# Performance work log

Hardware: AMD Instinct MI355X
Metric: run time of the kernel (lower is better)

## Reference

```python
import jax, jax.numpy as jnp
import numpy as np

NUM_USERS = 50000
NUM_ITEMS = 50000
N_NODES = NUM_USERS + NUM_ITEMS
DIM_FEAT = 256
HID = 128
EMB = 128
K = 3
N_EDGES = 1_600_000


def setup_inputs() -> dict:
    key = jax.random.key(0)
    ks = jax.random.split(key, 16)

    def xavier(k, shape):
        fan_in, fan_out = shape[-2], shape[-1]
        std = float(np.sqrt(2.0 / (fan_in + fan_out)))
        return jax.random.normal(k, shape, dtype=jnp.float32) * std

    return {
        "feat": jax.random.normal(ks[0], (NUM_ITEMS, DIM_FEAT), dtype=jnp.float32),
        "node_emb": jax.random.normal(ks[1], (N_NODES, EMB), dtype=jnp.float32),
        "src": jax.random.randint(ks[2], (N_EDGES,), 0, N_NODES, dtype=jnp.int32),
        "dst": jax.random.randint(ks[3], (N_EDGES,), 0, N_NODES, dtype=jnp.int32),
        "user_feat_emb": xavier(ks[4], (NUM_USERS, HID)),
        "trans_w": xavier(ks[5], (DIM_FEAT, HID)),
        "trans_b": jnp.zeros((HID,), dtype=jnp.float32),
        # layer 0: hidden->hidden; layers 1,2: emb->emb. hidden==emb so stack.
        "ws": xavier(ks[6], (K, HID, HID)),
        "des_w": xavier(ks[7], (K, HID, EMB)),
        "des_b": jnp.zeros((K, EMB), dtype=jnp.float32),
        # concat=True: outs[i] takes [h | u] of width hidden+emb
        "out_w": xavier(ks[8], (K, HID + EMB, EMB)),
        "out_b": jnp.zeros((K, EMB), dtype=jnp.float32),
    }


def reference(feat, node_emb, src, dst, user_feat_emb,
              trans_w, trans_b, ws, des_w, des_b, out_w, out_b):
    # feat = trans(feat); concat user embeddings; L2-normalize rows
    x = feat @ trans_w + trans_b                      # [num_items, HID]
    x = jnp.concatenate([user_feat_emb, x], axis=0)   # [N, HID]
    norm = jnp.linalg.norm(x, axis=1, keepdims=True)
    x = x / jnp.maximum(norm, 1e-12)

    lrelu = jax.nn.leaky_relu  # slope 0.01, matches F.leaky_relu default
    for i in range(K):
        # g.func(x, W): sparse adjacency aggregation (sum over in-edges) then dense W
        agg = jax.ops.segment_sum(x[src], dst, num_segments=N_NODES)  # [N, HID]
        h = lrelu(agg @ ws[i])                                        # [N, HID]
        u = lrelu(h @ des_w[i] + des_b[i] + node_emb)                 # [N, EMB]
        x = lrelu(jnp.concatenate([h, u], axis=1) @ out_w[i] + out_b[i])
    return x, user_feat_emb
```

## Files before the change

kernel.cpp:

```cpp
#include <hip/hip_runtime.h>

#define NN 100000
#define NU 50000
#define NI 50000
#define NE 1600000
#define NSLICE 5
#define SLICEW 20000

typedef unsigned short u16;
typedef unsigned int u32;

typedef __attribute__((ext_vector_type(8))) short s16x8;
typedef __attribute__((ext_vector_type(4))) float f32x4;
typedef __attribute__((ext_vector_type(4))) unsigned short us4;

__device__ __forceinline__ float bf2f(u16 u){
  union { u32 i; float f; } v; v.i = ((u32)u) << 16; return v.f;
}
__device__ __forceinline__ u16 f2bf(float f){
  union { float f; u32 i; } v; v.f = f;
  u32 u = v.i;
  return (u16)((u + 0x7FFFu + ((u >> 16) & 1u)) >> 16);
}
__device__ __forceinline__ u32 pack2(float lo, float hi){
  return (u32)f2bf(lo) | ((u32)f2bf(hi) << 16);
}
__device__ __forceinline__ float lrelu(float x){ return x > 0.f ? x : 0.01f * x; }
__device__ __forceinline__ float san(float v){
  union { float f; u32 i; } u; u.f = v;
  return ((u.i & 0x7F800000u) == 0x7F800000u) ? 0.f : v;
}

__global__ __launch_bounds__(256) void transpose_weights(
    const float* __restrict__ trans_w, const float* __restrict__ wsw,
    const float* __restrict__ desw, const float* __restrict__ outw,
    u16* __restrict__ Ttw, u16* __restrict__ Tw, u16* __restrict__ Td, u16* __restrict__ To)
{
  __shared__ u16 L[128][136];
  int b = blockIdx.x, t = threadIdx.x;
  const float* src; u16* dst; int stride;
  if (b < 2)      { src = trans_w + b*16384;        dst = Ttw + b*128;          stride = 256; }
  else if (b < 5) { int i = b-2; src = wsw  + i*16384; dst = Tw + i*16384;      stride = 128; }
  else if (b < 8) { int i = b-5; src = desw + i*16384; dst = Td + i*16384;      stride = 128; }
  else            { int i = (b-8)>>1, h = (b-8)&1;
                    src = outw + i*32768 + h*16384;    dst = To + i*32768 + h*128; stride = 256; }
  #pragma unroll
  for (int p = 0; p < 8; p++){
    int fi = (p*256 + t)*8;
    int r = fi >> 7, c = fi & 127;
    f32x4 v0 = *(const f32x4*)(src + r*128 + c);
    f32x4 v1 = *(const f32x4*)(src + r*128 + c + 4);
    L[c+0][r] = f2bf(san(v0.x)); L[c+1][r] = f2bf(san(v0.y));
    L[c+2][r] = f2bf(san(v0.z)); L[c+3][r] = f2bf(san(v0.w));
    L[c+4][r] = f2bf(san(v1.x)); L[c+5][r] = f2bf(san(v1.y));
    L[c+6][r] = f2bf(san(v1.z)); L[c+7][r] = f2bf(san(v1.w));
  }
  __syncthreads();
  #pragma unroll
  for (int p = 0; p < 8; p++){
    int fi = (p*256 + t)*8;
    int n = fi >> 7, k = fi & 127;
    us4 o0, o1;
    o0.x = L[n][k+0]; o0.y = L[n][k+1]; o0.z = L[n][k+2]; o0.w = L[n][k+3];
    o1.x = L[n][k+4]; o1.y = L[n][k+5]; o1.z = L[n][k+6]; o1.w = L[n][k+7];
    *(us4*)(dst + (size_t)n*stride + k)     = o0;
    *(us4*)(dst + (size_t)n*stride + k + 4) = o1;
  }
}

__global__ __launch_bounds__(256) void norm_users(const float* __restrict__ ufe, u16* __restrict__ X)
{
  int gid = blockIdx.x*256 + threadIdx.x;
  int row = gid >> 6, lane = gid & 63;
  float2 v = *(const float2*)(ufe + (size_t)row*128 + lane*2);
  float a = san(v.x), b = san(v.y);
  float ss = a*a + b*b;
  #pragma unroll
  for (int off = 32; off; off >>= 1) ss += __shfl_xor(ss, off, 64);
  float inv = 1.0f / fmaxf(sqrtf(ss), 1e-12f);
  *(u32*)(X + (size_t)row*128 + lane*2) = pack2(a*inv, b*inv);
}

__global__ __launch_bounds__(256) void trans_items(
    const float* __restrict__ feat, const u16* __restrict__ Ttw,
    const float* __restrict__ tb, u16* __restrict__ X)
{
  __shared__ u16 Af[128][136];
  __shared__ u16 Wl[128][136];
  __shared__ float rowss[128][9];
  __shared__ float rnorm[128];

  int t = threadIdx.x;
  int r0 = blockIdx.x * 128;
  int w = t >> 6, lane = t & 63;
  int l15 = lane & 15, q = lane >> 4;
  int m0 = (w & 1) * 64, n0 = (w >> 1) * 64;

  f32x4 acc[4][4];
  #pragma unroll
  for (int mi = 0; mi < 4; mi++)
    #pragma unroll
    for (int ni = 0; ni < 4; ni++){ acc[mi][ni].x = 0.f; acc[mi][ni].y = 0.f; acc[mi][ni].z = 0.f; acc[mi][ni].w = 0.f; }

  for (int half = 0; half < 2; half++){
    __syncthreads();
    #pragma unroll
    for (int p = 0; p < 8; p++){
      int fi = (p*256 + t)*8;
      int r = fi >> 7, c = fi & 127;
      int row = r0 + r;
      us4 o0 = {0,0,0,0}, o1 = {0,0,0,0};
      if (row < NI){
        f32x4 v0 = *(const f32x4*)(feat + (size_t)row*256 + half*128 + c);
        f32x4 v1 = *(const f32x4*)(feat + (size_t)row*256 + half*128 + c + 4);
        o0.x = f2bf(san(v0.x)); o0.y = f2bf(san(v0.y)); o0.z = f2bf(san(v0.z)); o0.w = f2bf(san(v0.w));
        o1.x = f2bf(san(v1.x)); o1.y = f2bf(san(v1.y)); o1.z = f2bf(san(v1.z)); o1.w = f2bf(san(v1.w));
      }
      *(us4*)&Af[r][c]     = o0;
      *(us4*)&Af[r][c + 4] = o1;
      *(us4*)&Wl[r][c]     = *(const us4*)(Ttw + (size_t)r*256 + half*128 + c);
      *(us4*)&Wl[r][c + 4] = *(const us4*)(Ttw + (size_t)r*256 + half*128 + c + 4);
    }
    __syncthreads();
    #pragma unroll
    for (int kc = 0; kc < 128; kc += 32){
      s16x8 afr[4], bfr[4];
      #pragma unroll
      for (int mi = 0; mi < 4; mi++) afr[mi] = *(const s16x8*)&Wl[m0 + 16*mi + l15][kc + 8*q];
      #pragma unroll
      for (int ni = 0; ni < 4; ni++) bfr[ni] = *(const s16x8*)&Af[n0 + 16*ni + l15][kc + 8*q];
      #pragma unroll
      for (int mi = 0; mi < 4; mi++)
        #pragma unroll
        for (int ni = 0; ni < 4; ni++)
          acc[mi][ni] = __builtin_amdgcn_mfma_f32_16x16x32_bf16(afr[mi], bfr[ni], acc[mi][ni], 0, 0, 0);
    }
  }

  float bias[4][4];
  #pragma unroll
  for (int mi = 0; mi < 4; mi++){
    int c0 = m0 + 16*mi + 4*q;
    f32x4 bv = *(const f32x4*)(tb + c0);
    bias[mi][0] = san(bv.x); bias[mi][1] = san(bv.y); bias[mi][2] = san(bv.z); bias[mi][3] = san(bv.w);
  }
  #pragma unroll
  for (int ni = 0; ni < 4; ni++){
    float ss = 0.f;
    #pragma unroll
    for (int mi = 0; mi < 4; mi++){
      float v0 = acc[mi][ni].x + bias[mi][0];
      float v1 = acc[mi][ni].y + bias[mi][1];
      float v2 = acc[mi][ni].z + bias[mi][2];
      float v3 = acc[mi][ni].w + bias[mi][3];
      ss += v0*v0 + v1*v1 + v2*v2 + v3*v3;
    }
    rowss[n0 + 16*ni + l15][(w & 1)*4 + q] = ss;
  }
  __syncthreads();
  if (t < 128){
    float s = 0.f;
    #pragma unroll
    for (int j = 0; j < 8; j++) s += rowss[t][j];
    rnorm[t] = 1.0f / fmaxf(sqrtf(s), 1e-12f);
  }
  __syncthreads();
  #pragma unroll
  for (int mi = 0; mi < 4; mi++){
    int c0 = m0 + 16*mi + 4*q;
    #pragma unroll
    for (int ni = 0; ni < 4; ni++){
      int r = n0 + 16*ni + l15;
      int row = r0 + r;
      if (row < NI){
        float inv = rnorm[r];
        us4 o;
        o.x = f2bf((acc[mi][ni].x + bias[mi][0]) * inv);
        o.y = f2bf((acc[mi][ni].y + bias[mi][1]) * inv);
        o.z = f2bf((acc[mi][ni].z + bias[mi][2]) * inv);
        o.w = f2bf((acc[mi][ni].w + bias[mi][3]) * inv);
        *(us4*)(X + (size_t)(NU + row)*128 + c0) = o;
      }
    }
  }
}

__global__ void zero_int(int* __restrict__ p, int n){
  int i = blockIdx.x*256 + threadIdx.x;
  if (i < n) p[i] = 0;
}
__global__ void hist_k(const int* __restrict__ dst, int* __restrict__ counts){
  int e = blockIdx.x*256 + threadIdx.x;
  if (e < NE){
    int d = dst[e];
    d = min(max(d, 0), NN - 1);
    atomicAdd(&counts[d], 1);
  }
}
__global__ __launch_bounds__(1024) void scan_k(const int* __restrict__ counts, int* __restrict__ row_ptr){
  __shared__ int lds[1024];
  __shared__ int carry;
  int t = threadIdx.x;
  if (t == 0) carry = 0;
  __syncthreads();
  for (int base = 0; base < NN; base += 4096){
    int idx = base + t*4;
    int4 v = {0,0,0,0};
    if (idx < NN) v = *(const int4*)(counts + idx);
    int s = v.x + v.y + v.z + v.w;
    lds[t] = s;
    __syncthreads();
    for (int off = 1; off < 1024; off <<= 1){
      int add = (t >= off) ? lds[t - off] : 0;
      __syncthreads();
      lds[t] += add;
      __syncthreads();
    }
    int incl = lds[t];
    int total = lds[1023];
    int run = carry;
    if (idx < NN){
      int e0 = run + incl - s;
      int4 o;
      o.x = e0; o.y = e0 + v.x; o.z = o.y + v.y; o.w = o.z + v.z;
      *(int4*)(row_ptr + idx) = o;
    }
    __syncthreads();
    if (t == 0) carry = run + total;
    __syncthreads();
  }
}

__global__ __launch_bounds__(256) void fill_slice(
    const int* __restrict__ src, const int* __restrict__ dst,
    int* __restrict__ row_ptr, int* __restrict__ esrc, int d0, int d1)
{
  int e = blockIdx.x*256 + threadIdx.x;
  if (e < NE){
    int d = dst[e];
    if (d >= d0 && d < d1){
      d = min(max(d, 0), NN - 1);
      int pos = atomicAdd(&row_ptr[d], 1);
      pos = min(max(pos, 0), NE - 1);
      esrc[pos] = src[e];
    }
  }
}

__global__ __launch_bounds__(256) void aggregate(
    const u16* __restrict__ X, const int* __restrict__ row_ptr,
    const int* __restrict__ esrc, u16* __restrict__ AGG)
{
  int gid = blockIdx.x*256 + threadIdx.x;
  int v = gid >> 6, lane = gid & 63;
  int sub = lane >> 4, li = lane & 15;
  int jb = (v == 0) ? 0 : row_ptr[v - 1];
  int je = row_ptr[v];
  jb = min(max(jb, 0), NE);
  je = min(max(je, jb), NE);

  float a0=0.f,a1=0.f,a2=0.f,a3=0.f,a4=0.f,a5=0.f,a6=0.f,a7=0.f;

  int j = jb + sub;
  for (; j + 4 < je; j += 8){
    int s0 = esrc[j];     s0 = min(max(s0, 0), NN - 1);
    int s1 = esrc[j + 4]; s1 = min(max(s1, 0), NN - 1);
    uint4 p0 = *(const uint4*)(X + (size_t)s0*128 + li*8);
    uint4 p1 = *(const uint4*)(X + (size_t)s1*128 + li*8);
    a0 += bf2f((u16)(p0.x & 0xFFFF)); a1 += bf2f((u16)(p0.x >> 16));
    a2 += bf2f((u16)(p0.y & 0xFFFF)); a3 += bf2f((u16)(p0.y >> 16));
    a4 += bf2f((u16)(p0.z & 0xFFFF)); a5 += bf2f((u16)(p0.z >> 16));
    a6 += bf2f((u16)(p0.w & 0xFFFF)); a7 += bf2f((u16)(p0.w >> 16));
    a0 += bf2f((u16)(p1.x & 0xFFFF)); a1 += bf2f((u16)(p1.x >> 16));
    a2 += bf2f((u16)(p1.y & 0xFFFF)); a3 += bf2f((u16)(p1.y >> 16));
    a4 += bf2f((u16)(p1.z & 0xFFFF)); a5 += bf2f((u16)(p1.z >> 16));
    a6 += bf2f((u16)(p1.w & 0xFFFF)); a7 += bf2f((u16)(p1.w >> 16));
  }
  for (; j < je; j += 4){
    int s0 = esrc[j]; s0 = min(max(s0, 0), NN - 1);
    uint4 p0 = *(const uint4*)(X + (size_t)s0*128 + li*8);
    a0 += bf2f((u16)(p0.x & 0xFFFF)); a1 += bf2f((u16)(p0.x >> 16));
    a2 += bf2f((u16)(p0.y & 0xFFFF)); a3 += bf2f((u16)(p0.y >> 16));
    a4 += bf2f((u16)(p0.z & 0xFFFF)); a5 += bf2f((u16)(p0.z >> 16));
    a6 += bf2f((u16)(p0.w & 0xFFFF)); a7 += bf2f((u16)(p0.w >> 16));
  }

  a0 += __shfl_xor(a0, 16, 64); a0 += __shfl_xor(a0, 32, 64);
  a1 += __shfl_xor(a1, 16, 64); a1 += __shfl_xor(a1, 32, 64);
  a2 += __shfl_xor(a2, 16, 64); a2 += __shfl_xor(a2, 32, 64);
  a3 += __shfl_xor(a3, 16, 64); a3 += __shfl_xor(a3, 32, 64);
  a4 += __shfl_xor(a4, 16, 64); a4 += __shfl_xor(a4, 32, 64);
  a5 += __shfl_xor(a5, 16, 64); a5 += __shfl_xor(a5, 32, 64);
  a6 += __shfl_xor(a6, 16, 64); a6 += __shfl_xor(a6, 32, 64);
  a7 += __shfl_xor(a7, 16, 64); a7 += __shfl_xor(a7, 32, 64);

  if (sub == 0){
    uint4 o;
    o.x = pack2(a0, a1); o.y = pack2(a2, a3);
    o.z = pack2(a4, a5); o.w = pack2(a6, a7);
    *(uint4*)(AGG + (size_t)v*128 + li*8) = o;
  }
}

__global__ __launch_bounds__(256, 2) void layer_fused(
    const u16* __restrict__ AGG, const float* __restrict__ nembF,
    const u16* __restrict__ Twi, const u16* __restrict__ Tdi,
    const float* __restrict__ dbF, const u16* __restrict__ Toi,
    const float* __restrict__ obF, u16* __restrict__ XoutB,
    float* __restrict__ XoutF, int last)
{
  __shared__ u16 Ab[128][136];
  __shared__ u16 Hb[128][136];

  int t = threadIdx.x;
  int r0 = blockIdx.x * 128;
  int w = t >> 6, lane = t & 63;
  int l15 = lane & 15, q = lane >> 4;
  int m0 = (w & 1) * 64, n0 = (w >> 1) * 64;

  f32x4 acc[4][4];

#define ZERO_ACC() \
  { _Pragma("unroll") for (int mi = 0; mi < 4; mi++) \
      { _Pragma("unroll") for (int ni = 0; ni < 4; ni++) \
        { acc[mi][ni].x = 0.f; acc[mi][ni].y = 0.f; acc[mi][ni].z = 0.f; acc[mi][ni].w = 0.f; } } }

#define GEMMG(BARR, WBASE, WSTRIDE, WKOFF) \
  { s16x8 afr[4][4]; \
    _Pragma("unroll") for (int mi = 0; mi < 4; mi++) \
      { _Pragma("unroll") for (int kk = 0; kk < 4; kk++) \
          afr[mi][kk] = *(const s16x8*)((WBASE) + (size_t)(m0 + 16*mi + l15)*(WSTRIDE) + (WKOFF) + kk*32 + 8*q); } \
    _Pragma("unroll") for (int kk = 0; kk < 4; kk++){ \
      s16x8 bfr[4]; \
      _Pragma("unroll") for (int ni = 0; ni < 4; ni++) bfr[ni] = *(const s16x8*)&BARR[n0 + 16*ni + l15][kk*32 + 8*q]; \
      _Pragma("unroll") for (int mi = 0; mi < 4; mi++) \
        { _Pragma("unroll") for (int ni = 0; ni < 4; ni++) \
          acc[mi][ni] = __builtin_amdgcn_mfma_f32_16x16x32_bf16(afr[mi][kk], bfr[ni], acc[mi][ni], 0, 0, 0); } } }

  #pragma unroll
  for (int p = 0; p < 8; p++){
    int fi = (p*256 + t)*8;
    int r = fi >> 7, c = fi & 127;
    int row = r0 + r;
    us4 o0 = {0,0,0,0}, o1 = {0,0,0,0};
    if (row < NN){
      o0 = *(const us4*)(AGG + (size_t)row*128 + c);
      o1 = *(const us4*)(AGG + (size_t)row*128 + c + 4);
    }
    *(us4*)&Ab[r][c]     = o0;
    *(us4*)&Ab[r][c + 4] = o1;
  }
  __syncthreads();

  ZERO_ACC();
  GEMMG(Ab, Twi, 128, 0);

  #pragma unroll
  for (int mi = 0; mi < 4; mi++){
    #pragma unroll
    for (int ni = 0; ni < 4; ni++){
      us4 o;
      o.x = f2bf(lrelu(acc[mi][ni].x));
      o.y = f2bf(lrelu(acc[mi][ni].y));
      o.z = f2bf(lrelu(acc[mi][ni].z));
      o.w = f2bf(lrelu(acc[mi][ni].w));
      *(us4*)&Hb[n0 + 16*ni + l15][m0 + 16*mi + 4*q] = o;
    }
  }
  __syncthreads();

  ZERO_ACC();
  GEMMG(Hb, Tdi, 128, 0);

  #pragma unroll
  for (int mi = 0; mi < 4; mi++){
    int c0 = m0 + 16*mi + 4*q;
    f32x4 dbv = *(const f32x4*)(dbF + c0);
    float db0 = san(dbv.x), db1 = san(dbv.y), db2 = san(dbv.z), db3 = san(dbv.w);
    #pragma unroll
    for (int ni = 0; ni < 4; ni++){
      int r = n0 + 16*ni + l15;
      int row = r0 + r;
      float e0 = 0.f, e1 = 0.f, e2 = 0.f, e3 = 0.f;
      if (row < NN){
        f32x4 nev = *(const f32x4*)(nembF + (size_t)row*128 + c0);
        e0 = san(nev.x); e1 = san(nev.y); e2 = san(nev.z); e3 = san(nev.w);
      }
      us4 o;
      o.x = f2bf(lrelu(acc[mi][ni].x + db0 + e0));
      o.y = f2bf(lrelu(acc[mi][ni].y + db1 + e1));
      o.z = f2bf(lrelu(acc[mi][ni].z + db2 + e2));
      o.w = f2bf(lrelu(acc[mi][ni].w + db3 + e3));
      *(us4*)&Ab[r][c0] = o;
    }
  }
  __syncthreads();

  ZERO_ACC();
  GEMMG(Hb, Toi, 256, 0);
  GEMMG(Ab, Toi, 256, 128);

  #pragma unroll
  for (int mi = 0; mi < 4; mi++){
    int c0 = m0 + 16*mi + 4*q;
    f32x4 obv = *(const f32x4*)(obF + c0);
    float b0 = san(obv.x), b1 = san(obv.y), b2 = san(obv.z), b3 = san(obv.w);
    #pragma unroll
    for (int ni = 0; ni < 4; ni++){
      int r = n0 + 16*ni + l15;
      int row = r0 + r;
      if (row < NN){
        if (last){
          f32x4 o;
          o.x = lrelu(acc[mi][ni].x + b0);
          o.y = lrelu(acc[mi][ni].y + b1);
          o.z = lrelu(acc[mi][ni].z + b2);
          o.w = lrelu(acc[mi][ni].w + b3);
          *(f32x4*)(XoutF + (size_t)row*128 + c0) = o;
        } else {
          us4 o;
          o.x = f2bf(lrelu(acc[mi][ni].x + b0));
          o.y = f2bf(lrelu(acc[mi][ni].y + b1));
          o.z = f2bf(lrelu(acc[mi][ni].z + b2));
          o.w = f2bf(lrelu(acc[mi][ni].w + b3));
          *(us4*)(XoutB + (size_t)row*128 + c0) = o;
        }
      }
    }
  }
#undef ZERO_ACC
#undef GEMMG
}

__global__ void copy_ufe(const float4* __restrict__ s, float4* __restrict__ d, int n){
  int i = blockIdx.x*256 + threadIdx.x;
  if (i < n){
    float4 v = s[i];
    v.x = san(v.x); v.y = san(v.y); v.z = san(v.z); v.w = san(v.w);
    d[i] = v;
  }
}

extern "C" void kernel_launch(void* const* d_in, const int* in_sizes, int n_in,
                              void* d_out, int out_size, void* d_ws, size_t ws_size,
                              hipStream_t stream)
{
  const float* feat = (const float*)d_in[0];
  const float* nemb = (const float*)d_in[1];
  const int*   src  = (const int*)d_in[2];
  const int*   dst  = (const int*)d_in[3];
  const float* ufe  = (const float*)d_in[4];
  const float* tw   = (const float*)d_in[5];
  const float* tb   = (const float*)d_in[6];
  const float* wsw  = (const float*)d_in[7];
  const float* desw = (const float*)d_in[8];
  const float* desb = (const float*)d_in[9];
  const float* outw = (const float*)d_in[10];
  const float* outb = (const float*)d_in[11];

  float* out  = (float*)d_out;
  float* outU = out + (size_t)NN*128;

  u16* X = (u16*)out;

  char* p = (char*)d_ws;
  u16*   AGG = (u16*)p;    p += (size_t)NN*128*2;
  u16*   Ttw = (u16*)p;    p += (size_t)2*16384*2;
  u16*   Tw  = (u16*)p;    p += (size_t)3*16384*2;
  u16*   Td  = (u16*)p;    p += (size_t)3*16384*2;
  u16*   To  = (u16*)p;    p += (size_t)3*32768*2;
  int* row_ptr = (int*)p;  p += (size_t)100004*4;
  int* counts  = (int*)p;  p += (size_t)100000*4;
  int* esrc    = (int*)p;  p += (size_t)NE*4;

  transpose_weights<<<14, 256, 0, stream>>>(tw, wsw, desw, outw, Ttw, Tw, Td, To);
  norm_users<<<NU/4, 256, 0, stream>>>(ufe, X);
  trans_items<<<(NI + 127)/128, 256, 0, stream>>>(feat, Ttw, tb, X);

  zero_int<<<(NN + 255)/256, 256, 0, stream>>>(counts, NN);
  hist_k<<<(NE + 255)/256, 256, 0, stream>>>(dst, counts);
  scan_k<<<1, 1024, 0, stream>>>(counts, row_ptr);
  for (int s = 0; s < NSLICE; s++){
    fill_slice<<<(NE + 255)/256, 256, 0, stream>>>(src, dst, row_ptr, esrc,
        s*SLICEW, (s == NSLICE-1) ? NN : (s+1)*SLICEW);
  }

  for (int i = 0; i < 3; i++){
    aggregate<<<NN/4, 256, 0, stream>>>(X, row_ptr, esrc, AGG);
    layer_fused<<<(NN + 127)/128, 256, 0, stream>>>(AGG, nemb,
        Tw + (size_t)i*16384, Td + (size_t)i*16384, desb + (size_t)i*128,
        To + (size_t)i*32768, outb + (size_t)i*128, X, out, (i == 2) ? 1 : 0);
  }
  copy_ufe<<<(NU*128/4 + 255)/256, 256, 0, stream>>>((const float4*)ufe, (float4*)outU, NU*128/4);
}
```

Before: 782.5 us.

## Shrink GEMM row tiles, pre-convert node_emb to bf16, warp-scan, deeper gather unroll

Several independent changes. layer_fused and trans_items now use 64-row tiles with launch bounds of 4 blocks, and trans_items reads weight fragments straight from global memory instead of staging them in LDS; this lowers LDS and register use so more blocks fit per CU. node_emb is converted once to bf16 into the user-output region, so each layer reads half the bytes, at the cost of bf16 rounding on that term. The scan kernel replaces its barrier-heavy LDS Hillis-Steele loop with wave shuffles, and the aggregate gather loop is unrolled to four outstanding row loads.

```diff
diff --git a/kernel.cpp b/kernel.cpp
--- a/kernel.cpp
+++ b/kernel.cpp
@@ -68,6 +68,20 @@
   }
 }
 
+__global__ __launch_bounds__(256) void conv_nemb(
+    const float* __restrict__ nemb, u16* __restrict__ nembB)
+{
+  int i = blockIdx.x*256 + threadIdx.x;
+  size_t off = (size_t)i * 8;
+  f32x4 v0 = *(const f32x4*)(nemb + off);
+  f32x4 v1 = *(const f32x4*)(nemb + off + 4);
+  us4 o0, o1;
+  o0.x = f2bf(san(v0.x)); o0.y = f2bf(san(v0.y)); o0.z = f2bf(san(v0.z)); o0.w = f2bf(san(v0.w));
+  o1.x = f2bf(san(v1.x)); o1.y = f2bf(san(v1.y)); o1.z = f2bf(san(v1.z)); o1.w = f2bf(san(v1.w));
+  *(us4*)(nembB + off)     = o0;
+  *(us4*)(nembB + off + 4) = o1;
+}
+
 __global__ __launch_bounds__(256) void norm_users(const float* __restrict__ ufe, u16* __restrict__ X)
 {
   int gid = blockIdx.x*256 + threadIdx.x;
@@ -81,31 +95,30 @@
   *(u32*)(X + (size_t)row*128 + lane*2) = pack2(a*inv, b*inv);
 }
 
-__global__ __launch_bounds__(256) void trans_items(
+__global__ __launch_bounds__(256, 4) void trans_items(
     const float* __restrict__ feat, const u16* __restrict__ Ttw,
     const float* __restrict__ tb, u16* __restrict__ X)
 {
-  __shared__ u16 Af[128][136];
-  __shared__ u16 Wl[128][136];
-  __shared__ float rowss[128][9];
-  __shared__ float rnorm[128];
+  __shared__ u16 Af[64][136];
+  __shared__ float rowss[64][8];
+  __shared__ float rnorm[64];
 
   int t = threadIdx.x;
-  int r0 = blockIdx.x * 128;
+  int r0 = blockIdx.x * 64;
   int w = t >> 6, lane = t & 63;
   int l15 = lane & 15, q = lane >> 4;
-  int m0 = (w & 1) * 64, n0 = (w >> 1) * 64;
-
-  f32x4 acc[4][4];
+  int m0 = (w & 1) * 64, n0 = (w >> 1) * 32;
+
+  f32x4 acc[4][2];
   #pragma unroll
   for (int mi = 0; mi < 4; mi++)
     #pragma unroll
-    for (int ni = 0; ni < 4; ni++){ acc[mi][ni].x = 0.f; acc[mi][ni].y = 0.f; acc[mi][ni].z = 0.f; acc[mi][ni].w = 0.f; }
+    for (int ni = 0; ni < 2; ni++){ acc[mi][ni].x = 0.f; acc[mi][ni].y = 0.f; acc[mi][ni].z = 0.f; acc[mi][ni].w = 0.f; }
 
   for (int half = 0; half < 2; half++){
     __syncthreads();
     #pragma unroll
-    for (int p = 0; p < 8; p++){
+    for (int p = 0; p < 4; p++){
       int fi = (p*256 + t)*8;
       int r = fi >> 7, c = fi & 127;
       int row = r0 + r;
@@ -118,21 +131,20 @@
       }
       *(us4*)&Af[r][c]     = o0;
       *(us4*)&Af[r][c + 4] = o1;
-      *(us4*)&Wl[r][c]     = *(const us4*)(Ttw + (size_t)r*256 + half*128 + c);
-      *(us4*)&Wl[r][c + 4] = *(const us4*)(Ttw + (size_t)r*256 + half*128 + c + 4);
     }
     __syncthreads();
     #pragma unroll
     for (int kc = 0; kc < 128; kc += 32){
-      s16x8 afr[4], bfr[4];
+      s16x8 afr[4], bfr[2];
       #pragma unroll
-      for (int mi = 0; mi < 4; mi++) afr[mi] = *(const s16x8*)&Wl[m0 + 16*mi + l15][kc + 8*q];
+      for (int mi = 0; mi < 4; mi++)
+        afr[mi] = *(const s16x8*)(Ttw + (size_t)(m0 + 16*mi + l15)*256 + half*128 + kc + 8*q);
       #pragma unroll
-      for (int ni = 0; ni < 4; ni++) bfr[ni] = *(const s16x8*)&Af[n0 + 16*ni + l15][kc + 8*q];
+      for (int ni = 0; ni < 2; ni++) bfr[ni] = *(const s16x8*)&Af[n0 + 16*ni + l15][kc + 8*q];
       #pragma unroll
       for (int mi = 0; mi < 4; mi++)
         #pragma unroll
-        for (int ni = 0; ni < 4; ni++)
+        for (int ni = 0; ni < 2; ni++)
           acc[mi][ni] = __builtin_amdgcn_mfma_f32_16x16x32_bf16(afr[mi], bfr[ni], acc[mi][ni], 0, 0, 0);
     }
   }
@@ -145,7 +157,7 @@
     bias[mi][0] = san(bv.x); bias[mi][1] = san(bv.y); bias[mi][2] = san(bv.z); bias[mi][3] = san(bv.w);
   }
   #pragma unroll
-  for (int ni = 0; ni < 4; ni++){
+  for (int ni = 0; ni < 2; ni++){
     float ss = 0.f;
     #pragma unroll
     for (int mi = 0; mi < 4; mi++){
@@ -158,7 +170,7 @@
     rowss[n0 + 16*ni + l15][(w & 1)*4 + q] = ss;
   }
   __syncthreads();
-  if (t < 128){
+  if (t < 64){
     float s = 0.f;
     #pragma unroll
     for (int j = 0; j < 8; j++) s += rowss[t][j];
@@ -169,7 +181,7 @@
   for (int mi = 0; mi < 4; mi++){
     int c0 = m0 + 16*mi + 4*q;
     #pragma unroll
-    for (int ni = 0; ni < 4; ni++){
+    for (int ni = 0; ni < 2; ni++){
       int r = n0 + 16*ni + l15;
       int row = r0 + r;
       if (row < NI){
@@ -198,35 +210,44 @@
   }
 }
 __global__ __launch_bounds__(1024) void scan_k(const int* __restrict__ counts, int* __restrict__ row_ptr){
-  __shared__ int lds[1024];
-  __shared__ int carry;
+  __shared__ int wsum[16];
+  __shared__ int woff[16];
+  __shared__ int tot;
   int t = threadIdx.x;
-  if (t == 0) carry = 0;
-  __syncthreads();
+  int lane = t & 63, wid = t >> 6;
+  int carry = 0;
   for (int base = 0; base < NN; base += 4096){
     int idx = base + t*4;
     int4 v = {0,0,0,0};
     if (idx < NN) v = *(const int4*)(counts + idx);
-    int s = v.x + v.y + v.z + v.w;
-    lds[t] = s;
+    int s4 = v.x + v.y + v.z + v.w;
+    int s = s4;
+    #pragma unroll
+    for (int off = 1; off < 64; off <<= 1){
+      int u = __shfl_up(s, off, 64);
+      if (lane >= off) s += u;
+    }
+    if (lane == 63) wsum[wid] = s;
     __syncthreads();
-    for (int off = 1; off < 1024; off <<= 1){
-      int add = (t >= off) ? lds[t - off] : 0;
-      __syncthreads();
-      lds[t] += add;
-      __syncthreads();
-    }
-    int incl = lds[t];
-    int total = lds[1023];
-    int run = carry;
+    if (t < 16){
+      int ws = wsum[t];
+      int wscan = ws;
+      #pragma unroll
+      for (int off = 1; off < 16; off <<= 1){
+        int u = __shfl_up(wscan, off, 64);
+        if (t >= off) wscan += u;
+      }
+      woff[t] = wscan - ws;
+      if (t == 15) tot = wscan;
+    }
+    __syncthreads();
     if (idx < NN){
-      int e0 = run + incl - s;
+      int e0 = carry + woff[wid] + (s - s4);
       int4 o;
       o.x = e0; o.y = e0 + v.x; o.z = o.y + v.y; o.w = o.z + v.z;
       *(int4*)(row_ptr + idx) = o;
     }
-    __syncthreads();
-    if (t == 0) carry = run + total;
+    carry += tot;
     __syncthreads();
   }
 }
@@ -247,6 +268,12 @@
   }
 }
 
+#define ACC8(P) \
+  a0 += bf2f((u16)(P.x & 0xFFFF)); a1 += bf2f((u16)(P.x >> 16)); \
+  a2 += bf2f((u16)(P.y & 0xFFFF)); a3 += bf2f((u16)(P.y >> 16)); \
+  a4 += bf2f((u16)(P.z & 0xFFFF)); a5 += bf2f((u16)(P.z >> 16)); \
+  a6 += bf2f((u16)(P.w & 0xFFFF)); a7 += bf2f((u16)(P.w >> 16));
+
 __global__ __launch_bounds__(256) void aggregate(
     const u16* __restrict__ X, const int* __restrict__ row_ptr,
     const int* __restrict__ esrc, u16* __restrict__ AGG)
@@ -262,27 +289,28 @@
   float a0=0.f,a1=0.f,a2=0.f,a3=0.f,a4=0.f,a5=0.f,a6=0.f,a7=0.f;
 
   int j = jb + sub;
+  for (; j + 12 < je; j += 16){
+    int s0 = esrc[j];      s0 = min(max(s0, 0), NN - 1);
+    int s1 = esrc[j + 4];  s1 = min(max(s1, 0), NN - 1);
+    int s2 = esrc[j + 8];  s2 = min(max(s2, 0), NN - 1);
+    int s3 = esrc[j + 12]; s3 = min(max(s3, 0), NN - 1);
+    uint4 p0 = *(const uint4*)(X + (size_t)s0*128 + li*8);
+    uint4 p1 = *(const uint4*)(X + (size_t)s1*128 + li*8);
+    uint4 p2 = *(const uint4*)(X + (size_t)s2*128 + li*8);
+    uint4 p3 = *(const uint4*)(X + (size_t)s3*128 + li*8);
+    ACC8(p0); ACC8(p1); ACC8(p2); ACC8(p3);
+  }
   for (; j + 4 < je; j += 8){
     int s0 = esrc[j];     s0 = min(max(s0, 0), NN - 1);
     int s1 = esrc[j + 4]; s1 = min(max(s1, 0), NN - 1);
     uint4 p0 = *(const uint4*)(X + (size_t)s0*128 + li*8);
     uint4 p1 = *(const uint4*)(X + (size_t)s1*128 + li*8);
-    a0 += bf2f((u16)(p0.x & 0xFFFF)); a1 += bf2f((u16)(p0.x >> 16));
-    a2 += bf2f((u16)(p0.y & 0xFFFF)); a3 += bf2f((u16)(p0.y >> 16));
-    a4 += bf2f((u16)(p0.z & 0xFFFF)); a5 += bf2f((u16)(p0.z >> 16));
-    a6 += bf2f((u16)(p0.w & 0xFFFF)); a7 += bf2f((u16)(p0.w >> 16));
-    a0 += bf2f((u16)(p1.x & 0xFFFF)); a1 += bf2f((u16)(p1.x >> 16));
-    a2 += bf2f((u16)(p1.y & 0xFFFF)); a3 += bf2f((u16)(p1.y >> 16));
-    a4 += bf2f((u16)(p1.z & 0xFFFF)); a5 += bf2f((u16)(p1.z >> 16));
-    a6 += bf2f((u16)(p1.w & 0xFFFF)); a7 += bf2f((u16)(p1.w >> 16));
+    ACC8(p0); ACC8(p1);
   }
   for (; j < je; j += 4){
     int s0 = esrc[j]; s0 = min(max(s0, 0), NN - 1);
     uint4 p0 = *(const uint4*)(X + (size_t)s0*128 + li*8);
-    a0 += bf2f((u16)(p0.x & 0xFFFF)); a1 += bf2f((u16)(p0.x >> 16));
-    a2 += bf2f((u16)(p0.y & 0xFFFF)); a3 += bf2f((u16)(p0.y >> 16));
-    a4 += bf2f((u16)(p0.z & 0xFFFF)); a5 += bf2f((u16)(p0.z >> 16));
-    a6 += bf2f((u16)(p0.w & 0xFFFF)); a7 += bf2f((u16)(p0.w >> 16));
+    ACC8(p0);
   }
 
   a0 += __shfl_xor(a0, 16, 64); a0 += __shfl_xor(a0, 32, 64);
@@ -302,27 +330,27 @@
   }
 }
 
-__global__ __launch_bounds__(256, 2) void layer_fused(
-    const u16* __restrict__ AGG, const float* __restrict__ nembF,
+__global__ __launch_bounds__(256, 4) void layer_fused(
+    const u16* __restrict__ AGG, const u16* __restrict__ nembB,
     const u16* __restrict__ Twi, const u16* __restrict__ Tdi,
     const float* __restrict__ dbF, const u16* __restrict__ Toi,
     const float* __restrict__ obF, u16* __restrict__ XoutB,
     float* __restrict__ XoutF, int last)
 {
-  __shared__ u16 Ab[128][136];
-  __shared__ u16 Hb[128][136];
+  __shared__ u16 Ab[64][136];
+  __shared__ u16 Hb[64][136];
 
   int t = threadIdx.x;
-  int r0 = blockIdx.x * 128;
+  int r0 = blockIdx.x * 64;
   int w = t >> 6, lane = t & 63;
   int l15 = lane & 15, q = lane >> 4;
-  int m0 = (w & 1) * 64, n0 = (w >> 1) * 64;
-
-  f32x4 acc[4][4];
+  int m0 = (w & 1) * 64, n0 = (w >> 1) * 32;
+
+  f32x4 acc[4][2];
 
 #define ZERO_ACC() \
   { _Pragma("unroll") for (int mi = 0; mi < 4; mi++) \
-      { _Pragma("unroll") for (int ni = 0; ni < 4; ni++) \
+      { _Pragma("unroll") for (int ni = 0; ni < 2; ni++) \
         { acc[mi][ni].x = 0.f; acc[mi][ni].y = 0.f; acc[mi][ni].z = 0.f; acc[mi][ni].w = 0.f; } } }
 
 #define GEMMG(BARR, WBASE, WSTRIDE, WKOFF) \
@@ -331,14 +359,14 @@
       { _Pragma("unroll") for (int kk = 0; kk < 4; kk++) \
           afr[mi][kk] = *(const s16x8*)((WBASE) + (size_t)(m0 + 16*mi + l15)*(WSTRIDE) + (WKOFF) + kk*32 + 8*q); } \
     _Pragma("unroll") for (int kk = 0; kk < 4; kk++){ \
-      s16x8 bfr[4]; \
-      _Pragma("unroll") for (int ni = 0; ni < 4; ni++) bfr[ni] = *(const s16x8*)&BARR[n0 + 16*ni + l15][kk*32 + 8*q]; \
+      s16x8 bfr[2]; \
+      _Pragma("unroll") for (int ni = 0; ni < 2; ni++) bfr[ni] = *(const s16x8*)&BARR[n0 + 16*ni + l15][kk*32 + 8*q]; \
       _Pragma("unroll") for (int mi = 0; mi < 4; mi++) \
-        { _Pragma("unroll") for (int ni = 0; ni < 4; ni++) \
+        { _Pragma("unroll") for (int ni = 0; ni < 2; ni++) \
           acc[mi][ni] = __builtin_amdgcn_mfma_f32_16x16x32_bf16(afr[mi][kk], bfr[ni], acc[mi][ni], 0, 0, 0); } } }
 
   #pragma unroll
-  for (int p = 0; p < 8; p++){
+  for (int p = 0; p < 4; p++){
     int fi = (p*256 + t)*8;
     int r = fi >> 7, c = fi & 127;
     int row = r0 + r;
@@ -358,7 +386,7 @@
   #pragma unroll
   for (int mi = 0; mi < 4; mi++){
     #pragma unroll
-    for (int ni = 0; ni < 4; ni++){
+    for (int ni = 0; ni < 2; ni++){
       us4 o;
       o.x = f2bf(lrelu(acc[mi][ni].x));
       o.y = f2bf(lrelu(acc[mi][ni].y));
@@ -378,13 +406,13 @@
     f32x4 dbv = *(const f32x4*)(dbF + c0);
     float db0 = san(dbv.x), db1 = san(dbv.y), db2 = san(dbv.z), db3 = san(dbv.w);
     #pragma unroll
-    for (int ni = 0; ni < 4; ni++){
+    for (int ni = 0; ni < 2; ni++){
       int r = n0 + 16*ni + l15;
       int row = r0 + r;
       float e0 = 0.f, e1 = 0.f, e2 = 0.f, e3 = 0.f;
       if (row < NN){
-        f32x4 nev = *(const f32x4*)(nembF + (size_t)row*128 + c0);
-        e0 = san(nev.x); e1 = san(nev.y); e2 = san(nev.z); e3 = san(nev.w);
+        us4 ne = *(const us4*)(nembB + (size_t)row*128 + c0);
+        e0 = bf2f(ne.x); e1 = bf2f(ne.y); e2 = bf2f(ne.z); e3 = bf2f(ne.w);
       }
       us4 o;
       o.x = f2bf(lrelu(acc[mi][ni].x + db0 + e0));
@@ -406,7 +434,7 @@
     f32x4 obv = *(const f32x4*)(obF + c0);
     float b0 = san(obv.x), b1 = san(obv.y), b2 = san(obv.z), b3 = san(obv.w);
     #pragma unroll
-    for (int ni = 0; ni < 4; ni++){
+    for (int ni = 0; ni < 2; ni++){
       int r = n0 + 16*ni + l15;
       int row = r0 + r;
       if (row < NN){
@@ -462,6 +490,7 @@
   float* outU = out + (size_t)NN*128;
 
   u16* X = (u16*)out;
+  u16* nembB = (u16*)outU;
 
   char* p = (char*)d_ws;
   u16*   AGG = (u16*)p;    p += (size_t)NN*128*2;
@@ -474,8 +503,9 @@
   int* esrc    = (int*)p;  p += (size_t)NE*4;
 
   transpose_weights<<<14, 256, 0, stream>>>(tw, wsw, desw, outw, Ttw, Tw, Td, To);
+  conv_nemb<<<6250, 256, 0, stream>>>(nemb, nembB);
   norm_users<<<NU/4, 256, 0, stream>>>(ufe, X);
-  trans_items<<<(NI + 127)/128, 256, 0, stream>>>(feat, Ttw, tb, X);
+  trans_items<<<(NI + 63)/64, 256, 0, stream>>>(feat, Ttw, tb, X);
 
   zero_int<<<(NN + 255)/256, 256, 0, stream>>>(counts, NN);
   hist_k<<<(NE + 255)/256, 256, 0, stream>>>(dst, counts);
@@ -487,7 +517,7 @@
 
   for (int i = 0; i < 3; i++){
     aggregate<<<NN/4, 256, 0, stream>>>(X, row_ptr, esrc, AGG);
-    layer_fused<<<(NN + 127)/128, 256, 0, stream>>>(AGG, nemb,
+    layer_fused<<<(NN + 63)/64, 256, 0, stream>>>(AGG, nembB,
         Tw + (size_t)i*16384, Td + (size_t)i*16384, desb + (size_t)i*128,
         To + (size_t)i*32768, outb + (size_t)i*128, X, out, (i == 2) ? 1 : 0);
   }
```

New measurement: 797.3 us. About the same (+1.9%).
